# Kernel optimization log

Hardware: AMD Instinct MI355X
Metric: run time of the kernel (lower is better)

## Reference

```python
import jax, jax.numpy as jnp
import numpy as np

N = 100000
E = 1600000
IN_DIM, HID_DIM, OUT_DIM = 128, 64, 128


def glorot(key, shape):
    lim = float(np.sqrt(6.0 / (shape[0] + shape[1])))
    return jax.random.uniform(key, shape, jnp.float32, -lim, lim)


def setup_inputs() -> dict:
    key = jax.random.key(0)
    k1, k2, k3, k4, k5 = jax.random.split(key, 5)
    x = jax.random.normal(k1, (N, IN_DIM), jnp.float32)
    edge_index = jax.random.randint(k2, (2, E), 0, N, jnp.int64)
    edge_weight = jax.random.uniform(k3, (E,), jnp.float32)
    W1 = glorot(k4, (IN_DIM, HID_DIM))
    b1 = jnp.zeros((HID_DIM,), jnp.float32)
    W2 = glorot(k5, (HID_DIM, OUT_DIM))
    b2 = jnp.zeros((OUT_DIM,), jnp.float32)
    return {"x": x, "edge_index": edge_index, "edge_weight": edge_weight,
            "W1": W1, "b1": b1, "W2": W2, "b2": b2}


def gcn_norm(edge_index, edge_weight, num_nodes):
    # add self-loops with weight 1 (PyG GCNConv default)
    loops = jnp.arange(num_nodes, dtype=edge_index.dtype)
    row = jnp.concatenate([edge_index[0], loops])
    col = jnp.concatenate([edge_index[1], loops])
    w = jnp.concatenate([edge_weight, jnp.ones((num_nodes,), edge_weight.dtype)])
    deg = jax.ops.segment_sum(w, col, num_segments=num_nodes)  # in-degree of targets
    dinv = jnp.where(deg > 0, jax.lax.rsqrt(deg), 0.0)
    norm = dinv[row] * w * dinv[col]  # [E+N]
    return row, col, norm


def gcn_conv(x, row, col, norm, W, b, num_nodes):
    h = x @ W                                   # [N, D_out]
    msg = h[row] * norm[:, None]                # [E+N, D_out] gather + scale
    out = jax.ops.segment_sum(msg, col, num_segments=num_nodes)  # scatter-add
    return out + b


def reference(x, edge_index, edge_weight, W1, b1, W2, b2):
    row, col, norm = gcn_norm(edge_index, edge_weight, N)
    h = jax.nn.relu(gcn_conv(x, row, col, norm, W1, b1, N))
    out = gcn_conv(h, row, col, norm, W2, b2, N)
    return out
```

## Files before the change

kernel.cpp:

```cpp
#include <hip/hip_runtime.h>
#include <hip/hip_bf16.h>

typedef __hip_bfloat16 bf16;
typedef __attribute__((ext_vector_type(8))) short short8;
typedef __attribute__((ext_vector_type(4))) float f32x4;
typedef __attribute__((ext_vector_type(2))) unsigned uv2;
typedef __attribute__((ext_vector_type(4))) unsigned uv4;
union V8 { uint4 u; short8 v; };

__device__ __forceinline__ float bf2f(bf16 v) { return __bfloat162float(v); }
__device__ __forceinline__ float lo16(unsigned u) { return __uint_as_float((u & 0xffffu) << 16); }
__device__ __forceinline__ float hi16(unsigned u) { return __uint_as_float(u & 0xffff0000u); }
__device__ __forceinline__ unsigned short f2bfbits(float f) {
    return (unsigned short)(__hip_bfloat16_raw(__float2bfloat16(f)).x);
}
__device__ __forceinline__ unsigned pack2(float a, float b) {
    return (unsigned)f2bfbits(a) | ((unsigned)f2bfbits(b) << 16);
}

__device__ __forceinline__ float ldf(const void* p, size_t i, bool isbf) {
    return isbf ? bf2f(((const bf16*)p)[i]) : ((const float*)p)[i];
}
__device__ __forceinline__ int ldi(const void* p, size_t i, bool is64) {
    return is64 ? (int)((const long long*)p)[i] : ((const int*)p)[i];
}
__device__ __forceinline__ float sane(float v) {
    return (v == v && fabsf(v) < 1e30f) ? v : 0.f;
}

__device__ __forceinline__ uint2 nt_ld2(const uint2* p) {
    uv2 v = __builtin_nontemporal_load((const uv2*)p);
    return make_uint2(v.x, v.y);
}
__device__ __forceinline__ void nt_st4(uint4* p, uint4 v) {
    uv4 t; t.x = v.x; t.y = v.y; t.z = v.z; t.w = v.w;
    __builtin_nontemporal_store(t, (uv4*)p);
}

#define DC_CNT_SHIFT 44
#define DC_FIX_MASK  0xFFFFFFFFFFFULL
#define DC_FIX_SCALE 4194304.0f

__global__ void detect(const unsigned* __restrict__ w1w, const unsigned* __restrict__ eiw,
                       int* __restrict__ flags) {
    __shared__ int cnt[2];
    if (threadIdx.x < 2) cnt[threadIdx.x] = 0;
    __syncthreads();
    int c0 = 0;
    for (int i = threadIdx.x; i < 4096; i += 256) {
        unsigned u = w1w[i];
        unsigned e0 = (u >> 7) & 0xFFu, e1 = (u >> 23) & 0xFFu;
        if (e0 <= 125u && e1 <= 125u) c0++;
    }
    int c1 = 0;
    for (int i = threadIdx.x; i < 2048; i += 256)
        if (eiw[2 * i + 1] == 0u) c1++;
    atomicAdd(&cnt[0], c0);
    atomicAdd(&cnt[1], c1);
    __syncthreads();
    if (threadIdx.x == 0) {
        flags[0] = (cnt[0] >= 3072) ? 1 : 0;
        flags[1] = (cnt[1] >= 1024) ? 1 : 0;
    }
}

__global__ void initk(unsigned long long* __restrict__ dc, int* __restrict__ hist,
                      int* __restrict__ bcnt, int n, int initdc) {
    int i = blockIdx.x * blockDim.x + threadIdx.x;
    if (initdc && i < n) dc[i] = (unsigned long long)(1u << 22);
    if (i < 256) { hist[i] = 0; bcnt[i] = 0; }
}

__global__ void degcnt(const void* __restrict__ ei, const void* __restrict__ w,
                       unsigned long long* __restrict__ dc,
                       const int* __restrict__ flags, int e, int n) {
    const bool isbf = flags[0] != 0;
    const bool is64 = flags[1] != 0;
    int i = blockIdx.x * blockDim.x + threadIdx.x;
    if (i < e) {
        int c = ldi(ei, (size_t)e + i, is64);
        if ((unsigned)c < (unsigned)n) {
            float wv = sane(ldf(w, i, isbf));
            wv = fminf(fmaxf(wv, 0.f), 1024.f);
            unsigned long long pk = (1ULL << DC_CNT_SHIFT)
                                  + (unsigned long long)llrintf(wv * DC_FIX_SCALE);
            atomicAdd(&dc[c], pk);
        }
    }
}

__global__ __launch_bounds__(1024) void binA(const void* __restrict__ ei,
                                             const void* __restrict__ w,
                                             int* __restrict__ bcnt,
                                             uint2* __restrict__ stage,
                                             const int* __restrict__ flags,
                                             int e, int n, int k, int cap) {
    __shared__ uint2 recs[4096];
    __shared__ unsigned tgt[4096];
    __shared__ int lh[256], loff[256], lbase[256];
    const bool isbf = flags[0] != 0;
    const bool is64 = flags[1] != 0;
    const int t = threadIdx.x;
    if (t < 256) lh[t] = 0;
    __syncthreads();

    int b_[4], lr_[4], valid_[4];
    uint2 rec_[4];
    const int base = blockIdx.x * 4096;
#pragma unroll
    for (int u = 0; u < 4; ++u) {
        int i = base + u * 1024 + t;
        valid_[u] = 0;
        if (i < e) {
            int r = ldi(ei, (size_t)i, is64);
            int c = ldi(ei, (size_t)e + i, is64);
            if ((unsigned)c < (unsigned)n) {
                bool rv = (unsigned)r < (unsigned)n;
                float wv = rv ? sane(ldf(w, i, isbf)) : 0.f;
                int b = c >> k;
                unsigned cloc = (unsigned)(c - (b << k));
                rec_[u] = make_uint2((cloc << 20) | (rv ? (unsigned)r : 0u),
                                     __float_as_uint(wv));
                b_[u] = b;
                lr_[u] = atomicAdd(&lh[b], 1);
                valid_[u] = 1;
            }
        }
    }
    __syncthreads();

    if (t < 256) loff[t] = lh[t];
    __syncthreads();
    for (int off = 1; off < 256; off <<= 1) {
        int v = 0;
        if (t < 256 && t >= off) v = loff[t - off];
        __syncthreads();
        if (t < 256 && t >= off) loff[t] += v;
        __syncthreads();
    }
    if (t < 256) {
        int c = lh[t];
        loff[t] -= c;
        lbase[t] = (c > 0) ? atomicAdd(&bcnt[t], c) : 0;
    }
    __syncthreads();

#pragma unroll
    for (int u = 0; u < 4; ++u)
        if (valid_[u]) {
            int slot = loff[b_[u]] + lr_[u];
            recs[slot] = rec_[u];
            unsigned gi = (unsigned)(lbase[b_[u]] + lr_[u]);
            tgt[slot] = (gi < (unsigned)cap)
                          ? (unsigned)b_[u] * (unsigned)cap + gi
                          : 0xFFFFFFFFu;
        }
    __syncthreads();

    const int total = loff[255] + lh[255];
    for (int s = t; s < total; s += 1024) {
        unsigned g = tgt[s];
        if (g != 0xFFFFFFFFu) stage[g] = recs[s];
    }
}

__global__ __launch_bounds__(1024) void degcntB(const uint2* __restrict__ stage,
                                                const int* __restrict__ bcnt,
                                                unsigned long long* __restrict__ dc,
                                                int n, int k, int cap) {
    __shared__ unsigned long long dcl[4096];
    const int b  = blockIdx.x;
    const int lo = b << k;
    const int hi = min(n, lo + (1 << k));
    const int bs = hi - lo;
    const int t  = threadIdx.x;
    for (int j = t; j < bs; j += 1024)
        dcl[j] = (unsigned long long)(1u << 22);
    __syncthreads();
    const uint2* sb = stage + (size_t)b * cap;
    const int cnt_b = min(bcnt[b], cap);
    for (int s = t; s < cnt_b; s += 1024) {
        uint2 rec = sb[s];
        int cloc  = (int)(rec.x >> 20);
        float wv  = __uint_as_float(rec.y);
        wv = fminf(fmaxf(wv, 0.f), 1024.f);
        unsigned long long pk = (1ULL << DC_CNT_SHIFT)
                              + (unsigned long long)llrintf(wv * DC_FIX_SCALE);
        atomicAdd(&dcl[cloc], pk);
    }
    __syncthreads();
    for (int j = t; j < bs; j += 1024) dc[lo + j] = dcl[j];
}

__global__ __launch_bounds__(1024) void scan1(const unsigned long long* __restrict__ dc,
                                              int* __restrict__ rp,
                                              int* __restrict__ bsum, int n) {
    __shared__ int s[1024];
    int gid = blockIdx.x * 1024 + threadIdx.x;
    int v = (gid < n) ? (int)(dc[gid] >> DC_CNT_SHIFT) : 0;
    s[threadIdx.x] = v;
    __syncthreads();
    for (int off = 1; off < 1024; off <<= 1) {
        int t = 0;
        if (threadIdx.x >= off) t = s[threadIdx.x - off];
        __syncthreads();
        if (threadIdx.x >= off) s[threadIdx.x] += t;
        __syncthreads();
    }
    if (gid < n) rp[gid] = s[threadIdx.x] - v;
    if (threadIdx.x == 1023) bsum[blockIdx.x] = s[1023];
}

__global__ __launch_bounds__(1024) void scan2(const int* __restrict__ bsum,
                                              int* __restrict__ bsx, int nb) {
    __shared__ int s[1024];
    int v = (threadIdx.x < nb) ? bsum[threadIdx.x] : 0;
    s[threadIdx.x] = v;
    __syncthreads();
    for (int off = 1; off < 1024; off <<= 1) {
        int t = 0;
        if (threadIdx.x >= off) t = s[threadIdx.x - off];
        __syncthreads();
        if (threadIdx.x >= off) s[threadIdx.x] += t;
        __syncthreads();
    }
    if (threadIdx.x < nb) bsx[threadIdx.x] = s[threadIdx.x] - v;
}

__global__ __launch_bounds__(1024) void scan3(int* __restrict__ rp, int* __restrict__ cursor,
                                              const int* __restrict__ bsx,
                                              unsigned long long* __restrict__ dc,
                                              int* __restrict__ hist,
                                              int n, int e) {
    __shared__ int lh[256];
    const int t = threadIdx.x;
    if (t < 256) lh[t] = 0;
    __syncthreads();
    int i = blockIdx.x * 1024 + t;
    if (i < n) {
        int v = rp[i] + bsx[i >> 10];
        rp[i] = v;
        cursor[i] = v;
        unsigned long long dv = dc[i];
        int c = (int)(dv >> DC_CNT_SHIFT);
        float d = (float)(dv & DC_FIX_MASK) * (1.0f / DC_FIX_SCALE);
        float di = d > 0.f ? rsqrtf(d) : 0.f;
        dc[i] = (dv & ~DC_FIX_MASK) | (unsigned long long)__float_as_uint(di);
        atomicAdd(&lh[min(c, 255)], 1);
    }
    __syncthreads();
    if (t < 256) {
        int c = lh[t];
        if (c > 0) atomicAdd(&hist[t], c);
    }
    if (i == 0) rp[n] = e;
}

__global__ void fill(const void* __restrict__ ei, const void* __restrict__ w,
                     int* __restrict__ cursor, uint2* __restrict__ epack,
                     const int* __restrict__ flags, int e, int n) {
    const bool isbf = flags[0] != 0;
    const bool is64 = flags[1] != 0;
    int i = blockIdx.x * blockDim.x + threadIdx.x;
    if (i < e) {
        int r = ldi(ei, (size_t)i, is64);
        int c = ldi(ei, (size_t)e + i, is64);
        if ((unsigned)c < (unsigned)n) {
            bool rv = (unsigned)r < (unsigned)n;
            float wv = rv ? sane(ldf(w, i, isbf)) : 0.f;
            int pos = atomicAdd(&cursor[c], 1);
            epack[pos] = make_uint2(rv ? (unsigned)r : 0u, __float_as_uint(wv));
        }
    }
}

__global__ __launch_bounds__(1024) void fillB(const int* __restrict__ rp,
                                              const uint2* __restrict__ stage,
                                              const int* __restrict__ bcnt,
                                              uint2* __restrict__ epack,
                                              int n, int k, int cap) {
    __shared__ int ncur[4096];
    const int b  = blockIdx.x;
    const int lo = b << k;
    const int hi = min(n, lo + (1 << k));
    const int t  = threadIdx.x;
    for (int j = t; j < hi - lo; j += 1024) ncur[j] = rp[lo + j];
    __syncthreads();
    const uint2* sb = stage + (size_t)b * cap;
    const int cnt_b = min(bcnt[b], cap);
    for (int s = t; s < cnt_b; s += 1024) {
        uint2 rec = sb[s];
        int cloc  = (int)(rec.x >> 20);
        unsigned r = rec.x & 0xFFFFFu;
        int pos = atomicAdd(&ncur[cloc], 1);
        epack[pos] = make_uint2(r, rec.y);
    }
}

__global__ void hscan(const int* __restrict__ hist, int* __restrict__ hcur) {
    __shared__ int s[256];
    int v = hist[threadIdx.x];
    s[threadIdx.x] = v;
    __syncthreads();
    for (int off = 1; off < 256; off <<= 1) {
        int t = 0;
        if (threadIdx.x >= off) t = s[threadIdx.x - off];
        __syncthreads();
        if (threadIdx.x >= off) s[threadIdx.x] += t;
        __syncthreads();
    }
    hcur[threadIdx.x] = s[threadIdx.x] - v;
}

__global__ __launch_bounds__(1024) void sortk(const unsigned long long* __restrict__ dc,
                                              int* __restrict__ hcur,
                                              int* __restrict__ order, int n) {
    __shared__ int lh[256];
    __shared__ int lbase[256];
    const int t = threadIdx.x;
    for (int b = t; b < 256; b += 1024) lh[b] = 0;
    __syncthreads();
    const int i = blockIdx.x * 1024 + t;
    int b = 0, lrank = 0;
    if (i < n) {
        b = min((int)(dc[i] >> DC_CNT_SHIFT), 255);
        lrank = atomicAdd(&lh[b], 1);
    }
    __syncthreads();
    for (int bb = t; bb < 256; bb += 1024) {
        int c = lh[bb];
        lbase[bb] = (c > 0) ? atomicAdd(&hcur[bb], c) : 0;
    }
    __syncthreads();
    if (i < n) order[lbase[b] + lrank] = i;
}

__global__ __launch_bounds__(256) void gemm1_mfma(const void* __restrict__ x,
                                                  const void* __restrict__ W1,
                                                  const float* __restrict__ dinvp,
                                                  const int* __restrict__ flags,
                                                  unsigned short* __restrict__ G1,
                                                  int n) {
    const bool isbf = flags[0] != 0;
    __shared__ uint4 bfr[16 * 64];
    for (int idx = threadIdx.x; idx < 16 * 64; idx += 256) {
        int lane = idx & 63, fr = idx >> 6;
        int ct = fr >> 2, ks = fr & 3;
        int k0 = ks * 32 + (lane >> 4) * 8;
        int col = ct * 16 + (lane & 15);
        unsigned short h[8];
#pragma unroll
        for (int j = 0; j < 8; ++j)
            h[j] = f2bfbits(ldf(W1, (size_t)(k0 + j) * 64 + col, isbf));
        bfr[idx] = make_uint4((unsigned)h[0] | ((unsigned)h[1] << 16),
                              (unsigned)h[2] | ((unsigned)h[3] << 16),
                              (unsigned)h[4] | ((unsigned)h[5] << 16),
                              (unsigned)h[6] | ((unsigned)h[7] << 16));
    }
    __syncthreads();

    const int lane = threadIdx.x & 63;
    const int m = lane & 15, q = lane >> 4;
    const int wid = (blockIdx.x * 256 + threadIdx.x) >> 6;
    const int nw  = (gridDim.x * 256) >> 6;
    const int nchunk = (n + 15) >> 4;

    for (int ch = wid; ch < nchunk; ch += nw) {
        const int row0 = ch * 16;
        const int rA = min(row0 + m, n - 1);
        V8 a[4];
        if (isbf) {
            const uint4* xr = (const uint4*)((const bf16*)x + (size_t)rA * 128);
#pragma unroll
            for (int ks = 0; ks < 4; ++ks) a[ks].u = xr[ks * 4 + q];
        } else {
            const float* xr = (const float*)x + (size_t)rA * 128;
#pragma unroll
            for (int ks = 0; ks < 4; ++ks) {
                unsigned short h[8];
#pragma unroll
                for (int j = 0; j < 8; ++j) h[j] = f2bfbits(xr[ks * 32 + q * 8 + j]);
                a[ks].u = make_uint4((unsigned)h[0] | ((unsigned)h[1] << 16),
                                     (unsigned)h[2] | ((unsigned)h[3] << 16),
                                     (unsigned)h[4] | ((unsigned)h[5] << 16),
                                     (unsigned)h[6] | ((unsigned)h[7] << 16));
            }
        }
#pragma unroll
        for (int ct = 0; ct < 4; ++ct) {
            f32x4 acc = {0.f, 0.f, 0.f, 0.f};
#pragma unroll
            for (int ks = 0; ks < 4; ++ks) {
                V8 b; b.u = bfr[(ct * 4 + ks) * 64 + lane];
                acc = __builtin_amdgcn_mfma_f32_16x16x32_bf16(a[ks].v, b.v, acc, 0, 0, 0);
            }
#pragma unroll
            for (int r = 0; r < 4; ++r) {
                int row = row0 + q * 4 + r;
                if (row < n)
                    G1[(size_t)row * 64 + ct * 16 + m] = f2bfbits(dinvp[2 * (size_t)row] * acc[r]);
            }
        }
    }
}

__device__ __forceinline__ void gacc8(const int* __restrict__ rp,
                                      const uint2* __restrict__ epack,
                                      const uint4* __restrict__ Gv,
                                      int node, int sub, float acc[8]) {
    uint4 self = Gv[(size_t)node * 8 + sub];
    acc[0] = lo16(self.x); acc[1] = hi16(self.x);
    acc[2] = lo16(self.y); acc[3] = hi16(self.y);
    acc[4] = lo16(self.z); acc[5] = hi16(self.z);
    acc[6] = lo16(self.w); acc[7] = hi16(self.w);

    const int s0 = rp[node], s1 = rp[node + 1];
    const uint2 fb = make_uint2((unsigned)node, 0u);
    int idx = s0 + sub;
    uint2 ld = (idx < s1) ? nt_ld2(&epack[idx]) : fb;
    for (int base = s0; base < s1; base += 8) {
        int nidx = base + 8 + sub;
        uint2 nld = (nidx < s1) ? nt_ld2(&epack[nidx]) : fb;
        int rr[8]; float wv[8];
#pragma unroll
        for (int u = 0; u < 8; ++u) {
            rr[u] = __shfl((int)ld.x, u, 8);
            wv[u] = __uint_as_float((unsigned)__shfl((int)ld.y, u, 8));
        }
        uint4 gp[8];
#pragma unroll
        for (int u = 0; u < 8; ++u) gp[u] = Gv[(size_t)rr[u] * 8 + sub];
#pragma unroll
        for (int u = 0; u < 8; ++u) {
            acc[0] = fmaf(wv[u], lo16(gp[u].x), acc[0]);
            acc[1] = fmaf(wv[u], hi16(gp[u].x), acc[1]);
            acc[2] = fmaf(wv[u], lo16(gp[u].y), acc[2]);
            acc[3] = fmaf(wv[u], hi16(gp[u].y), acc[3]);
            acc[4] = fmaf(wv[u], lo16(gp[u].z), acc[4]);
            acc[5] = fmaf(wv[u], hi16(gp[u].z), acc[5]);
            acc[6] = fmaf(wv[u], lo16(gp[u].w), acc[6]);
            acc[7] = fmaf(wv[u], hi16(gp[u].w), acc[7]);
        }
        ld = nld;
    }
}

__global__ __launch_bounds__(256, 4) void agg1(const int* __restrict__ rp,
                                               const uint2* __restrict__ epack,
                                               const int* __restrict__ order,
                                               const uint4* __restrict__ G1v,
                                               const float* __restrict__ dinvp,
                                               const void* __restrict__ b1,
                                               const int* __restrict__ flags,
                                               uint4* __restrict__ G2v, int n) {
    const bool isbf = flags[0] != 0;
    const int sub = threadIdx.x & 7;
    const int g   = (blockIdx.x * 256 + threadIdx.x) >> 3;
    if (g >= n) return;
    const int node = order[g];

    float acc[8];
    gacc8(rp, epack, G1v, node, sub, acc);

    const float dv = dinvp[2 * (size_t)node];
    unsigned o[4];
#pragma unroll
    for (int t = 0; t < 4; ++t) {
        float h0 = dv * acc[2 * t]     + ldf(b1, 8 * sub + 2 * t, isbf);
        float h1 = dv * acc[2 * t + 1] + ldf(b1, 8 * sub + 2 * t + 1, isbf);
        h0 = h0 > 0.f ? h0 : 0.f;
        h1 = h1 > 0.f ? h1 : 0.f;
        o[t] = pack2(dv * h0, dv * h1);
    }
    nt_st4(&G2v[(size_t)node * 8 + sub], make_uint4(o[0], o[1], o[2], o[3]));
}

__global__ __launch_bounds__(256, 4) void agg2(const int* __restrict__ rp,
                                               const uint2* __restrict__ epack,
                                               const int* __restrict__ order,
                                               const uint4* __restrict__ G2v,
                                               const float* __restrict__ dinvp,
                                               uint4* __restrict__ Tv, int n) {
    const int sub = threadIdx.x & 7;
    const int g   = (blockIdx.x * 256 + threadIdx.x) >> 3;
    if (g >= n) return;
    const int node = order[g];

    float acc[8];
    gacc8(rp, epack, G2v, node, sub, acc);

    const float dv = dinvp[2 * (size_t)node];
    uint4 o;
    o.x = pack2(dv * acc[0], dv * acc[1]);
    o.y = pack2(dv * acc[2], dv * acc[3]);
    o.z = pack2(dv * acc[4], dv * acc[5]);
    o.w = pack2(dv * acc[6], dv * acc[7]);
    nt_st4(&Tv[(size_t)node * 8 + sub], o);
}

__global__ __launch_bounds__(256) void outgemm_mfma(const bf16* __restrict__ T,
                                                    const void* __restrict__ W2,
                                                    const void* __restrict__ b2,
                                                    const int* __restrict__ flags,
                                                    void* __restrict__ outp, int n) {
    const bool isbf = flags[0] != 0;
    __shared__ uint4 bfr[16 * 64];
    __shared__ float b2s[128];
    for (int idx = threadIdx.x; idx < 16 * 64; idx += 256) {
        int lane = idx & 63, fr = idx >> 6;
        int ct = fr >> 1, ks = fr & 1;
        int k0 = ks * 32 + (lane >> 4) * 8;
        int col = ct * 16 + (lane & 15);
        unsigned short h[8];
#pragma unroll
        for (int j = 0; j < 8; ++j)
            h[j] = f2bfbits(ldf(W2, (size_t)(k0 + j) * 128 + col, isbf));
        bfr[idx] = make_uint4((unsigned)h[0] | ((unsigned)h[1] << 16),
                              (unsigned)h[2] | ((unsigned)h[3] << 16),
                              (unsigned)h[4] | ((unsigned)h[5] << 16),
                              (unsigned)h[6] | ((unsigned)h[7] << 16));
    }
    for (int i = threadIdx.x; i < 128; i += 256) b2s[i] = ldf(b2, i, isbf);
    __syncthreads();

    const int lane = threadIdx.x & 63;
    const int m = lane & 15, q = lane >> 4;
    const int wid = (blockIdx.x * 256 + threadIdx.x) >> 6;
    const int nw  = (gridDim.x * 256) >> 6;
    const int nchunk = (n + 15) >> 4;

    for (int ch = wid; ch < nchunk; ch += nw) {
        const int row0 = ch * 16;
        const int rA = min(row0 + m, n - 1);
        const uint4* tr = (const uint4*)(T + (size_t)rA * 64);
        V8 a[2];
        a[0].u = tr[q];
        a[1].u = tr[4 + q];
#pragma unroll
        for (int ct = 0; ct < 8; ++ct) {
            f32x4 acc = {0.f, 0.f, 0.f, 0.f};
#pragma unroll
            for (int ks = 0; ks < 2; ++ks) {
                V8 b; b.u = bfr[(ct * 2 + ks) * 64 + lane];
                acc = __builtin_amdgcn_mfma_f32_16x16x32_bf16(a[ks].v, b.v, acc, 0, 0, 0);
            }
            const int col = ct * 16 + m;
            const float bb = b2s[col];
#pragma unroll
            for (int r = 0; r < 4; ++r) {
                int row = row0 + q * 4 + r;
                if (row < n) {
                    float o = acc[r] + bb;
                    if (isbf) ((bf16*)outp)[(size_t)row * 128 + col] = __float2bfloat16(o);
                    else      ((float*)outp)[(size_t)row * 128 + col] = o;
                }
            }
        }
    }
}

extern "C" void kernel_launch(void* const* d_in, const int* in_sizes, int n_in,
                              void* d_out, int out_size, void* d_ws, size_t ws_size,
                              hipStream_t stream) {
    const void* x  = d_in[0];
    const void* ei = d_in[1];
    const void* ew = d_in[2];
    const void* W1 = d_in[3];
    const void* b1 = d_in[4];
    const void* W2 = d_in[5];
    const void* b2 = d_in[6];

    const int n = in_sizes[0] / 128;
    const int e = in_sizes[2];
    const int nb = (n + 1023) / 1024;

    int*   flags  = (int*)d_ws;
    unsigned long long* dc = (unsigned long long*)((int*)d_ws + 8);
    int*   rp     = (int*)d_ws + 8 + 2 * (size_t)n;
    int*   cursor = rp + n + 1;
    int*   bsum   = cursor + n;
    int*   bsx    = bsum + 1024;
    int*   hist   = bsum + 512;
    int*   hcur   = bsx + 512;
    int*   bcnt   = bsx + 256;
    int*   order  = cursor;
    size_t w_off  = (size_t)(8 + 4 * (size_t)n + 1 + 2048);
    w_off = (w_off + 3) & ~(size_t)3;
    uint2*    epack = (uint2*)((int*)d_ws + w_off);
    size_t g_off = w_off + 2 * (size_t)e;
    g_off = (g_off + 3) & ~(size_t)3;
    unsigned* G1 = (unsigned*)d_ws + g_off;
    unsigned* G2 = G1 + (size_t)n * 32;

    const float* dinvp = (const float*)dc;
    uint2* stage = (uint2*)G1;

    int bs0 = (n + 255) / 256;
    int k = 0;
    while ((1 << k) < bs0) ++k;
    int beff = (n + (1 << k) - 1) >> k;
    int cap  = (int)((32 * (size_t)n) / (size_t)beff);
    size_t mean = ((size_t)e + beff - 1) / beff;
    bool fastfill = (n <= (1 << 18)) && (k <= 12) &&
                    ((size_t)cap >= mean + mean / 2 + 1024);

    detect<<<1, 256, 0, stream>>>((const unsigned*)W1, (const unsigned*)ei, flags);
    initk<<<(n + 255) / 256, 256, 0, stream>>>(dc, hist, bcnt, n, fastfill ? 0 : 1);
    if (fastfill) {
        binA<<<(e + 4095) / 4096, 1024, 0, stream>>>(ei, ew, bcnt, stage, flags, e, n, k, cap);
        degcntB<<<beff, 1024, 0, stream>>>(stage, bcnt, dc, n, k, cap);
    } else {
        degcnt<<<(e + 255) / 256, 256, 0, stream>>>(ei, ew, dc, flags, e, n);
    }
    scan1<<<nb, 1024, 0, stream>>>(dc, rp, bsum, n);
    scan2<<<1, 1024, 0, stream>>>(bsum, bsx, nb);
    scan3<<<nb, 1024, 0, stream>>>(rp, cursor, bsx, dc, hist, n, e);
    if (fastfill) {
        fillB<<<beff, 1024, 0, stream>>>(rp, stage, bcnt, epack, n, k, cap);
    } else {
        fill<<<(e + 255) / 256, 256, 0, stream>>>(ei, ew, cursor, epack, flags, e, n);
    }
    hscan<<<1, 256, 0, stream>>>(hist, hcur);
    sortk<<<nb, 1024, 0, stream>>>(dc, hcur, order, n);

    gemm1_mfma<<<192, 256, 0, stream>>>(x, W1, dinvp, flags, (unsigned short*)G1, n);
    agg1<<<(n * 8 + 255) / 256, 256, 0, stream>>>(rp, epack, order, (const uint4*)G1,
                                                  dinvp, b1, flags, (uint4*)G2, n);
    agg2<<<(n * 8 + 255) / 256, 256, 0, stream>>>(rp, epack, order, (const uint4*)G2,
                                                  dinvp, (uint4*)G1, n);
    outgemm_mfma<<<192, 256, 0, stream>>>((const bf16*)G1, W2, b2, flags, d_out, n);
}
```

Measured before the change: 369.5 us.

## Fold detect into init kernel, vectorize fp32 x loads, enlarge GEMM grids

Merges the single-block format-detection kernel into the init kernel, which removes one launch. The fp32 path of the first GEMM now loads rows with float4 vector loads instead of scalar loads. Both MFMA GEMM kernels get a grid sized from the row-chunk count, clamped to 192–2048 blocks, instead of a fixed 192. This gives more waves for latency hiding on the memory-bound GEMMs, at some cost in block scheduling overhead.

```diff
diff --git a/kernel.cpp b/kernel.cpp
--- a/kernel.cpp
+++ b/kernel.cpp
@@ -41,34 +41,34 @@
 #define DC_FIX_MASK  0xFFFFFFFFFFFULL
 #define DC_FIX_SCALE 4194304.0f
 
-__global__ void detect(const unsigned* __restrict__ w1w, const unsigned* __restrict__ eiw,
-                       int* __restrict__ flags) {
-    __shared__ int cnt[2];
-    if (threadIdx.x < 2) cnt[threadIdx.x] = 0;
-    __syncthreads();
-    int c0 = 0;
-    for (int i = threadIdx.x; i < 4096; i += 256) {
-        unsigned u = w1w[i];
-        unsigned e0 = (u >> 7) & 0xFFu, e1 = (u >> 23) & 0xFFu;
-        if (e0 <= 125u && e1 <= 125u) c0++;
-    }
-    int c1 = 0;
-    for (int i = threadIdx.x; i < 2048; i += 256)
-        if (eiw[2 * i + 1] == 0u) c1++;
-    atomicAdd(&cnt[0], c0);
-    atomicAdd(&cnt[1], c1);
-    __syncthreads();
-    if (threadIdx.x == 0) {
-        flags[0] = (cnt[0] >= 3072) ? 1 : 0;
-        flags[1] = (cnt[1] >= 1024) ? 1 : 0;
-    }
-}
-
 __global__ void initk(unsigned long long* __restrict__ dc, int* __restrict__ hist,
-                      int* __restrict__ bcnt, int n, int initdc) {
+                      int* __restrict__ bcnt, int n, int initdc,
+                      const unsigned* __restrict__ w1w, const unsigned* __restrict__ eiw,
+                      int* __restrict__ flags) {
     int i = blockIdx.x * blockDim.x + threadIdx.x;
     if (initdc && i < n) dc[i] = (unsigned long long)(1u << 22);
     if (i < 256) { hist[i] = 0; bcnt[i] = 0; }
+    if (blockIdx.x == 0) {
+        __shared__ int cnt[2];
+        if (threadIdx.x < 2) cnt[threadIdx.x] = 0;
+        __syncthreads();
+        int c0 = 0;
+        for (int j = threadIdx.x; j < 4096; j += 256) {
+            unsigned u = w1w[j];
+            unsigned e0 = (u >> 7) & 0xFFu, e1 = (u >> 23) & 0xFFu;
+            if (e0 <= 125u && e1 <= 125u) c0++;
+        }
+        int c1 = 0;
+        for (int j = threadIdx.x; j < 2048; j += 256)
+            if (eiw[2 * j + 1] == 0u) c1++;
+        atomicAdd(&cnt[0], c0);
+        atomicAdd(&cnt[1], c1);
+        __syncthreads();
+        if (threadIdx.x == 0) {
+            flags[0] = (cnt[0] >= 3072) ? 1 : 0;
+            flags[1] = (cnt[1] >= 1024) ? 1 : 0;
+        }
+    }
 }
 
 __global__ void degcnt(const void* __restrict__ ei, const void* __restrict__ w,
@@ -374,16 +374,13 @@
 #pragma unroll
             for (int ks = 0; ks < 4; ++ks) a[ks].u = xr[ks * 4 + q];
         } else {
-            const float* xr = (const float*)x + (size_t)rA * 128;
+            const float4* xr4 = (const float4*)((const float*)x + (size_t)rA * 128);
 #pragma unroll
             for (int ks = 0; ks < 4; ++ks) {
-                unsigned short h[8];
-#pragma unroll
-                for (int j = 0; j < 8; ++j) h[j] = f2bfbits(xr[ks * 32 + q * 8 + j]);
-                a[ks].u = make_uint4((unsigned)h[0] | ((unsigned)h[1] << 16),
-                                     (unsigned)h[2] | ((unsigned)h[3] << 16),
-                                     (unsigned)h[4] | ((unsigned)h[5] << 16),
-                                     (unsigned)h[6] | ((unsigned)h[7] << 16));
+                float4 v0 = xr4[ks * 8 + q * 2];
+                float4 v1 = xr4[ks * 8 + q * 2 + 1];
+                a[ks].u = make_uint4(pack2(v0.x, v0.y), pack2(v0.z, v0.w),
+                                     pack2(v1.x, v1.y), pack2(v1.z, v1.w));
             }
         }
 #pragma unroll
@@ -604,8 +601,13 @@
     bool fastfill = (n <= (1 << 18)) && (k <= 12) &&
                     ((size_t)cap >= mean + mean / 2 + 1024);
 
-    detect<<<1, 256, 0, stream>>>((const unsigned*)W1, (const unsigned*)ei, flags);
-    initk<<<(n + 255) / 256, 256, 0, stream>>>(dc, hist, bcnt, n, fastfill ? 0 : 1);
+    const int nchunk = (n + 15) >> 4;
+    int ggrid = (nchunk + 3) / 4;
+    if (ggrid > 2048) ggrid = 2048;
+    if (ggrid < 192)  ggrid = 192;
+
+    initk<<<(n + 255) / 256, 256, 0, stream>>>(dc, hist, bcnt, n, fastfill ? 0 : 1,
+                                               (const unsigned*)W1, (const unsigned*)ei, flags);
     if (fastfill) {
         binA<<<(e + 4095) / 4096, 1024, 0, stream>>>(ei, ew, bcnt, stage, flags, e, n, k, cap);
         degcntB<<<beff, 1024, 0, stream>>>(stage, bcnt, dc, n, k, cap);
@@ -623,10 +625,10 @@
     hscan<<<1, 256, 0, stream>>>(hist, hcur);
     sortk<<<nb, 1024, 0, stream>>>(dc, hcur, order, n);
 
-    gemm1_mfma<<<192, 256, 0, stream>>>(x, W1, dinvp, flags, (unsigned short*)G1, n);
+    gemm1_mfma<<<ggrid, 256, 0, stream>>>(x, W1, dinvp, flags, (unsigned short*)G1, n);
     agg1<<<(n * 8 + 255) / 256, 256, 0, stream>>>(rp, epack, order, (const uint4*)G1,
                                                   dinvp, b1, flags, (uint4*)G2, n);
     agg2<<<(n * 8 + 255) / 256, 256, 0, stream>>>(rp, epack, order, (const uint4*)G2,
                                                   dinvp, (uint4*)G1, n);
-    outgemm_mfma<<<192, 256, 0, stream>>>((const bf16*)G1, W2, b2, flags, d_out, n);
-}
+    outgemm_mfma<<<ggrid, 256, 0, stream>>>((const bf16*)G1, W2, b2, flags, d_out, n);
+}
```

Measured after the change: 350.6 us. 1.05x faster.
